# Kernel tuning notes

Measured on AMD Instinct MI355X. Metric: run time of the kernel, lower is better.

## Reference

```python
import jax, jax.numpy as jnp
import numpy as np
from jax import lax

N = 2048
D_ENC = 64      # conv channels
D = 512         # node embedding dim (resnet18 feature dim)
K = 5           # max_num_neighbors
L_LAYERS = 4    # num_layers
ARENA = 32.0    # positions scaled to [0, ARENA)^2
R2 = 2.0        # radius^2 = (sqrt(2))^2


def setup_inputs() -> dict:
    key = jax.random.key(0)
    ks = jax.random.split(key, 9)
    imgs = jax.random.normal(ks[0], (N, 3, 64, 64), dtype=jnp.float32)
    pos = jax.random.uniform(ks[1], (N, 2), dtype=jnp.float32)  # scaled by ARENA inside
    conv_w = jax.random.normal(ks[2], (D_ENC, 3, 7, 7), dtype=jnp.float32) * 0.05
    conv_b = jnp.zeros((D_ENC,), dtype=jnp.float32)
    proj_w = jax.random.normal(ks[3], (D_ENC, D), dtype=jnp.float32) * (1.0 / np.sqrt(D_ENC))
    proj_b = jnp.zeros((D,), dtype=jnp.float32)
    w_self = jax.random.normal(ks[4], (L_LAYERS, D, D), dtype=jnp.float32) * (1.0 / np.sqrt(D))
    w_nbr = jax.random.normal(ks[5], (L_LAYERS, D, D), dtype=jnp.float32) * (1.0 / np.sqrt(D))
    b_gnn = jnp.zeros((L_LAYERS, D), dtype=jnp.float32)
    return {"imgs": imgs, "pos": pos, "conv_w": conv_w, "conv_b": conv_b,
            "proj_w": proj_w, "proj_b": proj_b,
            "w_self": w_self, "w_nbr": w_nbr, "b_gnn": b_gnn}


def _encode(imgs, conv_w, conv_b, proj_w, proj_b):
    # conv 7x7 stride 2 + relu + global avg pool + linear -> [N, D]
    x = lax.conv_general_dilated(imgs, conv_w, window_strides=(2, 2), padding="SAME",
                                 dimension_numbers=("NCHW", "OIHW", "NCHW"))
    x = jax.nn.relu(x + conv_b[None, :, None, None])
    x = x.mean(axis=(2, 3))                      # [N, D_ENC]
    return jax.nn.relu(x @ proj_w + proj_b)      # [N, D]


def _radius_knn(pos):
    # radius graph with radius sqrt(2), no self loops, capped at K neighbors
    p = pos * ARENA                              # [N, 2]
    d2 = jnp.sum((p[:, None, :] - p[None, :, :]) ** 2, axis=-1)  # [N, N]
    invalid = (d2 > R2) | jnp.eye(N, dtype=bool)
    d2m = jnp.where(invalid, jnp.inf, d2)
    neg_vals, idx = lax.top_k(-d2m, K)           # K nearest within radius
    valid = jnp.isfinite(neg_vals)               # [N, K]
    return idx, valid


def reference(imgs, pos, conv_w, conv_b, proj_w, proj_b, w_self, w_nbr, b_gnn):
    h = _encode(imgs, conv_w, conv_b, proj_w, proj_b)   # [N, D]
    idx, valid = _radius_knn(pos)                        # [N, K], [N, K]
    vmask = valid.astype(h.dtype)                        # [N, K]
    denom = jnp.maximum(vmask.sum(axis=1, keepdims=True), 1.0)  # [N, 1]
    for l in range(L_LAYERS):
        nbr = h[idx] * vmask[:, :, None]                 # [N, K, D] gather
        agg = nbr.sum(axis=1) / denom                    # mean over valid neighbors
        h = jax.nn.relu(h @ w_self[l] + agg @ w_nbr[l] + b_gnn[l])
    return h
```

## Files before the change

### kernel.cpp

```cpp
#include <hip/hip_runtime.h>


#define NNODES 2048

typedef __attribute__((ext_vector_type(8))) _Float16 half8;
typedef __attribute__((ext_vector_type(16))) float f32x16;

__device__ inline uint pack2h(float x, float y) {
  ushort a = __builtin_bit_cast(ushort, (_Float16)x);
  ushort b = __builtin_bit_cast(ushort, (_Float16)y);
  return (uint)a | ((uint)b << 16);
}

__global__ __launch_bounds__(256) void setup_kernel(
    const float* __restrict__ conv_w, const float* __restrict__ wsrc_s,
    const float* __restrict__ wsrc_n, const float* __restrict__ pos,
    ushort* __restrict__ wfrag, ushort* __restrict__ wT,
    int* __restrict__ nbr, float* __restrict__ den, float* __restrict__ enc) {
  __shared__ float4 smem4[1040];
  const int bid = blockIdx.x;
  const int tid = threadIdx.x;

  if (bid < 48) {
    int i = bid * 256 + tid;
    int j = i & 7;
    int l = (i >> 3) & 63;
    int q = i >> 9;
    int kb = q % 12, ct = q / 12;
    int g = 2 * kb + (l >> 5);
    int c = 32 * ct + (l & 31);
    float val = 0.f;
    if (g < 21 && j < 7) val = conv_w[c * 147 + g * 7 + j];
    wfrag[i] = __builtin_bit_cast(ushort, (_Float16)val);
    return;
  }

  if (bid < 560) {
    float(*s)[65] = (float(*)[65])smem4;
    int bid2 = bid - 48;
    int m = bid2 >> 6, kt = (bid2 >> 3) & 7, nt = bid2 & 7;
    const float* in = (m < 4) ? (wsrc_s + m * 262144) : (wsrc_n + (m - 4) * 262144);
    ushort* out = wT + m * 262144;
    int k0 = kt << 6, n0 = nt << 6;
#pragma unroll
    for (int rep = 0; rep < 4; ++rep) {
      int row = (rep << 4) + (tid >> 4);
      int c4 = (tid & 15) << 2;
      float4 v = *(const float4*)&in[(k0 + row) * 512 + n0 + c4];
      s[row][c4] = v.x; s[row][c4 + 1] = v.y; s[row][c4 + 2] = v.z; s[row][c4 + 3] = v.w;
    }
    __syncthreads();
#pragma unroll
    for (int rep = 0; rep < 4; ++rep) {
      int n = (rep << 4) + (tid >> 4);
      int k4 = (tid & 15) << 2;
      ushort4 o;
      o.x = __builtin_bit_cast(ushort, (_Float16)s[k4 + 0][n]);
      o.y = __builtin_bit_cast(ushort, (_Float16)s[k4 + 1][n]);
      o.z = __builtin_bit_cast(ushort, (_Float16)s[k4 + 2][n]);
      o.w = __builtin_bit_cast(ushort, (_Float16)s[k4 + 3][n]);
      *(ushort4*)&out[(n0 + n) * 512 + k0 + k4] = o;
    }
    return;
  }

  {
    float* s_d2 = (float*)smem4;
    int* s_idx = (int*)(s_d2 + NNODES);
    int* s_cnt = (int*)(s_idx + NNODES);
    const int i = bid - 560;
    if (tid < 16) {
      float4 z4 = {0.f, 0.f, 0.f, 0.f};
      ((float4*)(enc + i * 64))[tid] = z4;
    }
    if (tid == 0) *s_cnt = 0;
    __syncthreads();
    const float px = pos[2 * i] * 32.f, py = pos[2 * i + 1] * 32.f;
#pragma unroll
    for (int r = 0; r < 8; ++r) {
      int j = tid + (r << 8);
      float2 q = ((const float2*)pos)[j];
      float dx = q.x * 32.f - px, dy = q.y * 32.f - py;
      float d2 = dx * dx + dy * dy;
      if (d2 <= 2.0f && j != i) {
        int slot = atomicAdd(s_cnt, 1);
        s_d2[slot] = d2;
        s_idx[slot] = j;
      }
    }
    __syncthreads();
    if (tid < 64) {
      const int lane = tid;
      const int cnt = *s_cnt;
      int nf = 0;
#pragma unroll
      for (int k = 0; k < 5; ++k) {
        float best = 1e30f;
        int bslot = 0x7fffffff;
        for (int e = lane; e < cnt; e += 64) {
          float d = s_d2[e];
          if (d < best) { best = d; bslot = e; }
        }
#pragma unroll
        for (int off = 1; off < 64; off <<= 1) {
          float od = __shfl_xor(best, off);
          int os = __shfl_xor(bslot, off);
          if (od < best || (od == best && os < bslot)) { best = od; bslot = os; }
        }
        bool got = (best < 1e30f);
        if (lane == 0) nbr[i * 5 + k] = got ? s_idx[bslot] : -1;
        if (got) { s_d2[bslot] = 1e30f; ++nf; }
      }
      if (lane == 0) den[i] = 1.f / (float)(nf > 0 ? nf : 1);
    }
  }
}

__global__ __launch_bounds__(256, 3) void conv_pool_kernel(
    const float* __restrict__ imgs, const ushort* __restrict__ wfrag,
    const float* __restrict__ cb, float* __restrict__ enc) {
  __shared__ int4 s_all[2599];
  ushort* s_img = (ushort*)s_all;
  const half8* swf8 = (const half8*)((char*)s_all + 15984);
  float* s_pool = (float*)((char*)s_all + 40560);

  const int n = blockIdx.x >> 1;
  const int r0half = blockIdx.x & 1;
  const int wy = 32 * r0half - 2;
  const int tid = threadIdx.x;
  const int lane = tid & 63;
  const int w = tid >> 6;
  const int hi = lane >> 5;
  const int lo = lane & 31;

  int4 z = {0, 0, 0, 0};
  for (int i = tid; i < 999; i += 256) s_all[i] = z;
  __syncthreads();

  const int4* wf4 = (const int4*)wfrag;
  int4* swf4 = (int4*)((char*)s_all + 15984);
#pragma unroll
  for (int r = 0; r < 6; ++r) swf4[tid + r * 256] = wf4[tid + r * 256];

  const float4* src = (const float4*)(imgs + (size_t)n * 12288);
  for (int i = tid; i < 1776; i += 256) {
    int ic = i / 592;
    int rem = i - ic * 592;
    int li = rem >> 4, xq = rem & 15;
    int iy = wy + li;
    if (iy >= 0 && iy < 64) {
      float4 v = src[(ic * 64 + iy) * 16 + xq];
      int d = (ic * 37 + li) * 72 + (xq << 2) + 2;
      ((uint*)s_img)[d >> 1] = pack2h(v.x, v.y);
      ((uint*)s_img)[(d >> 1) + 1] = pack2h(v.z, v.w);
    }
  }

  int aoff[12];
#pragma unroll
  for (int kb = 0; kb < 12; ++kb) {
    int g = 2 * kb + hi;
    if (g > 20) g = 20;
    int ic = g / 7, ky = g - ic * 7;
    aoff[kb] = (ic * 37 + ky) * 144 + 4 * lo + w * 1152;
  }
  const float bias0 = cb[lo];
  const float bias1 = cb[32 + lo];
  float pool0 = 0.f, pool1 = 0.f;
  __syncthreads();

  const char* sb = (const char*)s_img;
  union F { half8 v; uint u[4]; };

#define LOADF(F0, F1, B0, B1, KB, TPADD) do {                       \
    const char* p_ = sb + aoff[KB] + (TPADD);                       \
    F0.u[0] = *(const uint*)(p_);       F0.u[1] = *(const uint*)(p_ + 4);   \
    F0.u[2] = *(const uint*)(p_ + 8);   F0.u[3] = *(const uint*)(p_ + 12);  \
    F1.u[0] = *(const uint*)(p_ + 288); F1.u[1] = *(const uint*)(p_ + 292); \
    F1.u[2] = *(const uint*)(p_ + 296); F1.u[3] = *(const uint*)(p_ + 300); \
    B0 = swf8[(KB) * 64 + lane];        B1 = swf8[(12 + (KB)) * 64 + lane]; \
  } while (0)

#pragma unroll
  for (int tp = 0; tp < 2; ++tp) {
    const int tpadd = tp * 576;
    f32x16 a0 = {}, a1 = {}, a2 = {}, a3 = {};
    F f0a, f1a, f0b, f1b;
    half8 b0a, b1a, b0b, b1b;
    LOADF(f0a, f1a, b0a, b1a, 0, tpadd);
#pragma unroll
    for (int kb = 0; kb < 12; kb += 2) {
      LOADF(f0b, f1b, b0b, b1b, kb + 1, tpadd);
      a0 = __builtin_amdgcn_mfma_f32_32x32x16_f16(f0a.v, b0a, a0, 0, 0, 0);
      a1 = __builtin_amdgcn_mfma_f32_32x32x16_f16(f0a.v, b1a, a1, 0, 0, 0);
      a2 = __builtin_amdgcn_mfma_f32_32x32x16_f16(f1a.v, b0a, a2, 0, 0, 0);
      a3 = __builtin_amdgcn_mfma_f32_32x32x16_f16(f1a.v, b1a, a3, 0, 0, 0);
      if (kb + 2 < 12) LOADF(f0a, f1a, b0a, b1a, kb + 2, tpadd);
      a0 = __builtin_amdgcn_mfma_f32_32x32x16_f16(f0b.v, b0b, a0, 0, 0, 0);
      a1 = __builtin_amdgcn_mfma_f32_32x32x16_f16(f0b.v, b1b, a1, 0, 0, 0);
      a2 = __builtin_amdgcn_mfma_f32_32x32x16_f16(f1b.v, b0b, a2, 0, 0, 0);
      a3 = __builtin_amdgcn_mfma_f32_32x32x16_f16(f1b.v, b1b, a3, 0, 0, 0);
    }
    float s0 = 0.f, s1 = 0.f;
#pragma unroll
    for (int r = 0; r < 16; ++r) {
      s0 += fmaxf(a0[r] + bias0, 0.f) + fmaxf(a2[r] + bias0, 0.f);
      s1 += fmaxf(a1[r] + bias1, 0.f) + fmaxf(a3[r] + bias1, 0.f);
    }
    pool0 += s0;
    pool1 += s1;
  }
#undef LOADF

  pool0 += __shfl_xor(pool0, 32);
  pool1 += __shfl_xor(pool1, 32);
  if (lane < 32) {
    s_pool[w * 64 + lo] = pool0;
    s_pool[w * 64 + 32 + lo] = pool1;
  }
  __syncthreads();
  if (tid < 64) {
    float s = s_pool[tid] + s_pool[64 + tid] + s_pool[128 + tid] + s_pool[192 + tid];
    atomicAdd(&enc[n * 64 + tid], s * (1.f / 1024.f));
  }
}

__global__ __launch_bounds__(256) void proj_kernel(
    const float* __restrict__ enc, const float* __restrict__ pw,
    const float* __restrict__ pb, ushort* __restrict__ h16) {
  int c = ((blockIdx.x & 1) << 8) | threadIdx.x;
  int r0 = (blockIdx.x >> 1) << 3;
  float bias = pb[c];
  float acc[8];
#pragma unroll
  for (int r = 0; r < 8; ++r) acc[r] = bias;
#pragma unroll 4
  for (int k = 0; k < 64; ++k) {
    float w = pw[k * 512 + c];
#pragma unroll
    for (int r = 0; r < 8; ++r) acc[r] = fmaf(enc[(r0 + r) * 64 + k], w, acc[r]);
  }
#pragma unroll
  for (int r = 0; r < 8; ++r)
    h16[(r0 + r) * 512 + c] = __builtin_bit_cast(ushort, (_Float16)fmaxf(acc[r], 0.f));
}

__global__ __launch_bounds__(256) void gnn_gemm_kernel(
    const ushort* __restrict__ h16, const int* __restrict__ nbr,
    const float* __restrict__ den,
    const ushort* __restrict__ Ws, const ushort* __restrict__ Wn,
    const float* __restrict__ bias, ushort* __restrict__ hout,
    float* __restrict__ fout, int final_layer) {
  __shared__ ushort s_lds[2][16384];
  __shared__ int s_nbr[320];
  __shared__ float s_den[64];
  const int tid = threadIdx.x;
  const int lane = tid & 63;
  const int hi = lane >> 5, lo = lane & 31;
  const int wu = __builtin_amdgcn_readfirstlane(tid >> 6);
  const int wr = wu >> 1, wc = wu & 1;
  const int bm = blockIdx.x >> 3, bn = blockIdx.x & 7;
  const int r0 = bm << 6, c0 = bn << 6;

  if (tid < 80) ((int4*)s_nbr)[tid] = ((const int4*)(nbr + r0 * 5))[tid];
  else if (tid < 96) ((float4*)s_den)[tid - 80] = ((const float4*)(den + r0))[tid - 80];
  __syncthreads();

  const int grow = tid >> 2, gseg = tid & 3;
  int gj[5];
  uint gm[5];
#pragma unroll
  for (int k = 0; k < 5; ++k) {
    int j = s_nbr[grow * 5 + k];
    gm[k] = (j >= 0) ? 0xFFFFFFFFu : 0u;
    gj[k] = (j >= 0) ? j : 0;
  }
  half8 den8;
  {
    _Float16 dh = (_Float16)s_den[grow];
#pragma unroll
    for (int e = 0; e < 8; ++e) den8[e] = dh;
  }

  union GU { half8 v; uint u[4]; };
  GU ga[5][2];

  auto GATHER = [&](int it) {
    const ushort* hb = h16 + (it << 6) + gseg * 16;
#pragma unroll
    for (int k = 0; k < 5; ++k) {
      const half8* p = (const half8*)(hb + gj[k] * 512);
      ga[k][0].v = p[0];
      ga[k][1].v = p[1];
    }
  };
  auto COMBINE = [&](int buf) {
#pragma unroll
    for (int part = 0; part < 2; ++part) {
      GU t0, t1, t2, t3, t4;
#pragma unroll
      for (int j2 = 0; j2 < 4; ++j2) {
        t0.u[j2] = ga[0][part].u[j2] & gm[0];
        t1.u[j2] = ga[1][part].u[j2] & gm[1];
        t2.u[j2] = ga[2][part].u[j2] & gm[2];
        t3.u[j2] = ga[3][part].u[j2] & gm[3];
        t4.u[j2] = ga[4][part].u[j2] & gm[4];
      }
      half8 s = ((t0.v + t1.v) + (t2.v + t3.v)) + t4.v;
      s = s * den8;
      *(half8*)&s_lds[buf][4096 + (2 * gseg + part) * 512 + grow * 8] = s;
    }
  };
  auto STAGE = [&](int buf, int it) {
    int k0 = it << 6;
    const ushort* ph = h16 + (r0 + lane) * 512 + k0 + 8 * wu;
    const ushort* ps = Ws + (c0 + lane) * 512 + k0 + 8 * wu;
    const ushort* pn = Wn + (c0 + lane) * 512 + k0 + 8 * wu;
    ushort* lb = &s_lds[buf][wu << 9];
#define GLDS(SRC, DST) __builtin_amdgcn_global_load_lds( \
      (const __attribute__((address_space(1))) void*)(SRC), \
      (__attribute__((address_space(3))) void*)(DST), 16, 0, 0)
    GLDS(ph, lb);            GLDS(ph + 32, lb + 2048);
    GLDS(ps, lb + 8192);     GLDS(ps + 32, lb + 10240);
    GLDS(pn, lb + 12288);    GLDS(pn + 32, lb + 14336);
#undef GLDS
  };

  f32x16 accS = {}, accN = {};
  GATHER(0);
  STAGE(0, 0);
  COMBINE(0);
  __syncthreads();
  int cur = 0;
  for (int it = 0; it < 8; ++it) {
    if (it < 7) {
      GATHER(it + 1);
      STAGE(cur ^ 1, it + 1);
    }
    const half8* pAh = (const half8*)&s_lds[cur][0];
    const half8* pAg = (const half8*)&s_lds[cur][4096];
    const half8* pBs = (const half8*)&s_lds[cur][8192];
    const half8* pBn = (const half8*)&s_lds[cur][12288];
#pragma unroll
    for (int ks = 0; ks < 4; ++ks) {
      int gi = (2 * ks + hi) * 64;
      half8 ah = pAh[gi + 32 * wr + lo];
      half8 bs = pBs[gi + 32 * wc + lo];
      accS = __builtin_amdgcn_mfma_f32_32x32x16_f16(ah, bs, accS, 0, 0, 0);
      half8 ag = pAg[gi + 32 * wr + lo];
      half8 bn2 = pBn[gi + 32 * wc + lo];
      accN = __builtin_amdgcn_mfma_f32_32x32x16_f16(ag, bn2, accN, 0, 0, 0);
    }
    if (it < 7) COMBINE(cur ^ 1);
    __syncthreads();
    cur ^= 1;
  }

  const int col = c0 + 32 * wc + lo;
  const float b = bias[col];
#pragma unroll
  for (int r = 0; r < 16; ++r) {
    int row = r0 + 32 * wr + (r & 3) + ((r >> 2) << 3) + (hi << 2);
    float v = fmaxf(accS[r] + accN[r] + b, 0.f);
    if (final_layer) fout[row * 512 + col] = v;
    else hout[row * 512 + col] = __builtin_bit_cast(ushort, (_Float16)v);
  }
}

extern "C" void kernel_launch(void* const* d_in, const int* in_sizes, int n_in,
                              void* d_out, int out_size, void* d_ws, size_t ws_size,
                              hipStream_t stream) {
  const float* imgs   = (const float*)d_in[0];
  const float* pos    = (const float*)d_in[1];
  const float* conv_w = (const float*)d_in[2];
  const float* conv_b = (const float*)d_in[3];
  const float* proj_w = (const float*)d_in[4];
  const float* proj_b = (const float*)d_in[5];
  const float* w_self = (const float*)d_in[6];
  const float* w_nbr  = (const float*)d_in[7];
  const float* b_gnn  = (const float*)d_in[8];

  char* ws = (char*)d_ws;
  ushort* wfrag = (ushort*)(ws);
  float*  enc   = (float*) (ws + 32768);
  ushort* h16a  = (ushort*)(ws + 557056);
  ushort* h16b  = (ushort*)(ws + 2654208);
  ushort* wT16  = (ushort*)(ws + 6848512);
  int*    nbr   = (int*)   (ws + 11042816);
  float*  den   = (float*) (ws + 11083776);

  setup_kernel<<<2608, 256, 0, stream>>>(conv_w, w_self, w_nbr, pos,
                                         wfrag, wT16, nbr, den, enc);
  conv_pool_kernel<<<2 * NNODES, 256, 0, stream>>>(imgs, wfrag, conv_b, enc);
  proj_kernel<<<512, 256, 0, stream>>>(enc, proj_w, proj_b, h16a);

  for (int l = 0; l < 4; ++l) {
    ushort* hin  = (l & 1) ? h16b : h16a;
    ushort* hnew = (l & 1) ? h16a : h16b;
    gnn_gemm_kernel<<<256, 256, 0, stream>>>(
        hin, nbr, den, wT16 + l * 262144, wT16 + (4 + l) * 262144,
        b_gnn + l * 512, hnew, (float*)d_out, (l == 3) ? 1 : 0);
  }
}
```

Before: 141.7 us.

## Split GNN GEMM K-loop across two wave groups with LDS reduction

The GNN layer kernel now launches 512 threads per block. Two groups of four waves each process half of the K dimension with their own double-buffered LDS stages, and the partial accumulators are reduced through LDS before the epilogue. The aim is more waves per block and a shorter serial K-loop, since only 256 blocks run on a GPU with many CUs. The cost is doubled LDS (128KB), which limits occupancy, plus an extra reduction barrier. Separately, the conv fragment loads are rewritten as 8-byte memcpy loads with an alignment hint so the compiler may emit wider LDS reads.

```diff
diff --git a/kernel.cpp b/kernel.cpp
--- a/kernel.cpp
+++ b/kernel.cpp
@@ -172,13 +172,14 @@
   const char* sb = (const char*)s_img;
   union F { half8 v; uint u[4]; };
 
-#define LOADF(F0, F1, B0, B1, KB, TPADD) do {                       \
-    const char* p_ = sb + aoff[KB] + (TPADD);                       \
-    F0.u[0] = *(const uint*)(p_);       F0.u[1] = *(const uint*)(p_ + 4);   \
-    F0.u[2] = *(const uint*)(p_ + 8);   F0.u[3] = *(const uint*)(p_ + 12);  \
-    F1.u[0] = *(const uint*)(p_ + 288); F1.u[1] = *(const uint*)(p_ + 292); \
-    F1.u[2] = *(const uint*)(p_ + 296); F1.u[3] = *(const uint*)(p_ + 300); \
-    B0 = swf8[(KB) * 64 + lane];        B1 = swf8[(12 + (KB)) * 64 + lane]; \
+#define LOADF(F0, F1, B0, B1, KB, TPADD) do {                                 \
+    const char* p_ = (const char*)__builtin_assume_aligned(                   \
+        sb + aoff[KB] + (TPADD), 4);                                          \
+    __builtin_memcpy(&F0.u[0], p_, 8);                                        \
+    __builtin_memcpy(&F0.u[2], p_ + 8, 8);                                    \
+    __builtin_memcpy(&F1.u[0], p_ + 288, 8);                                  \
+    __builtin_memcpy(&F1.u[2], p_ + 296, 8);                                  \
+    B0 = swf8[(KB) * 64 + lane];        B1 = swf8[(12 + (KB)) * 64 + lane];   \
   } while (0)
 
 #pragma unroll
@@ -245,28 +246,31 @@
     h16[(r0 + r) * 512 + c] = __builtin_bit_cast(ushort, (_Float16)fmaxf(acc[r], 0.f));
 }
 
-__global__ __launch_bounds__(256) void gnn_gemm_kernel(
+__global__ __launch_bounds__(512) void gnn_gemm_kernel(
     const ushort* __restrict__ h16, const int* __restrict__ nbr,
     const float* __restrict__ den,
     const ushort* __restrict__ Ws, const ushort* __restrict__ Wn,
     const float* __restrict__ bias, ushort* __restrict__ hout,
     float* __restrict__ fout, int final_layer) {
-  __shared__ ushort s_lds[2][16384];
+  __shared__ ushort s_lds[4][16384];
   __shared__ int s_nbr[320];
   __shared__ float s_den[64];
   const int tid = threadIdx.x;
   const int lane = tid & 63;
   const int hi = lane >> 5, lo = lane & 31;
-  const int wu = __builtin_amdgcn_readfirstlane(tid >> 6);
-  const int wr = wu >> 1, wc = wu & 1;
+  const int grp = tid >> 8;
+  const int wug = __builtin_amdgcn_readfirstlane((tid >> 6) & 3);
+  const int wr = wug >> 1, wc = wug & 1;
   const int bm = blockIdx.x >> 3, bn = blockIdx.x & 7;
   const int r0 = bm << 6, c0 = bn << 6;
+  const int itb = grp << 2;
 
   if (tid < 80) ((int4*)s_nbr)[tid] = ((const int4*)(nbr + r0 * 5))[tid];
   else if (tid < 96) ((float4*)s_den)[tid - 80] = ((const float4*)(den + r0))[tid - 80];
   __syncthreads();
 
-  const int grow = tid >> 2, gseg = tid & 3;
+  const int ltid = tid & 255;
+  const int grow = ltid >> 2, gseg = ltid & 3;
   int gj[5];
   uint gm[5];
 #pragma unroll
@@ -313,10 +317,10 @@
   };
   auto STAGE = [&](int buf, int it) {
     int k0 = it << 6;
-    const ushort* ph = h16 + (r0 + lane) * 512 + k0 + 8 * wu;
-    const ushort* ps = Ws + (c0 + lane) * 512 + k0 + 8 * wu;
-    const ushort* pn = Wn + (c0 + lane) * 512 + k0 + 8 * wu;
-    ushort* lb = &s_lds[buf][wu << 9];
+    const ushort* ph = h16 + (r0 + lane) * 512 + k0 + 8 * wug;
+    const ushort* ps = Ws + (c0 + lane) * 512 + k0 + 8 * wug;
+    const ushort* pn = Wn + (c0 + lane) * 512 + k0 + 8 * wug;
+    ushort* lb = &s_lds[buf][wug << 9];
 #define GLDS(SRC, DST) __builtin_amdgcn_global_load_lds( \
       (const __attribute__((address_space(1))) void*)(SRC), \
       (__attribute__((address_space(3))) void*)(DST), 16, 0, 0)
@@ -327,20 +331,21 @@
   };
 
   f32x16 accS = {}, accN = {};
-  GATHER(0);
-  STAGE(0, 0);
-  COMBINE(0);
+  GATHER(itb);
+  STAGE(itb == 0 ? 0 : 2, itb);
+  COMBINE(itb == 0 ? 0 : 2);
   __syncthreads();
   int cur = 0;
-  for (int it = 0; it < 8; ++it) {
-    if (it < 7) {
-      GATHER(it + 1);
-      STAGE(cur ^ 1, it + 1);
-    }
-    const half8* pAh = (const half8*)&s_lds[cur][0];
-    const half8* pAg = (const half8*)&s_lds[cur][4096];
-    const half8* pBs = (const half8*)&s_lds[cur][8192];
-    const half8* pBn = (const half8*)&s_lds[cur][12288];
+  const int bufbase = grp << 1;
+  for (int it = 0; it < 4; ++it) {
+    if (it < 3) {
+      GATHER(itb + it + 1);
+      STAGE(bufbase + (cur ^ 1), itb + it + 1);
+    }
+    const half8* pAh = (const half8*)&s_lds[bufbase + cur][0];
+    const half8* pAg = (const half8*)&s_lds[bufbase + cur][4096];
+    const half8* pBs = (const half8*)&s_lds[bufbase + cur][8192];
+    const half8* pBn = (const half8*)&s_lds[bufbase + cur][12288];
 #pragma unroll
     for (int ks = 0; ks < 4; ++ks) {
       int gi = (2 * ks + hi) * 64;
@@ -351,19 +356,28 @@
       half8 bn2 = pBn[gi + 32 * wc + lo];
       accN = __builtin_amdgcn_mfma_f32_32x32x16_f16(ag, bn2, accN, 0, 0, 0);
     }
-    if (it < 7) COMBINE(cur ^ 1);
+    if (it < 3) COMBINE(bufbase + (cur ^ 1));
     __syncthreads();
     cur ^= 1;
   }
 
-  const int col = c0 + 32 * wc + lo;
-  const float b = bias[col];
-#pragma unroll
-  for (int r = 0; r < 16; ++r) {
-    int row = r0 + 32 * wr + (r & 3) + ((r >> 2) << 3) + (hi << 2);
-    float v = fmaxf(accS[r] + accN[r] + b, 0.f);
-    if (final_layer) fout[row * 512 + col] = v;
-    else hout[row * 512 + col] = __builtin_bit_cast(ushort, (_Float16)v);
+  float* s_red = (float*)&s_lds[0][0];
+  if (grp == 1) {
+#pragma unroll
+    for (int r = 0; r < 16; ++r)
+      s_red[(ltid << 4) + r] = accS[r] + accN[r];
+  }
+  __syncthreads();
+  if (grp == 0) {
+    const int col = c0 + 32 * wc + lo;
+    const float b = bias[col];
+#pragma unroll
+    for (int r = 0; r < 16; ++r) {
+      int row = r0 + 32 * wr + (r & 3) + ((r >> 2) << 3) + (hi << 2);
+      float v = fmaxf(accS[r] + accN[r] + s_red[(ltid << 4) + r] + b, 0.f);
+      if (final_layer) fout[row * 512 + col] = v;
+      else hout[row * 512 + col] = __builtin_bit_cast(ushort, (_Float16)v);
+    }
   }
 }
 
@@ -397,7 +411,7 @@
   for (int l = 0; l < 4; ++l) {
     ushort* hin  = (l & 1) ? h16b : h16a;
     ushort* hnew = (l & 1) ? h16a : h16b;
-    gnn_gemm_kernel<<<256, 256, 0, stream>>>(
+    gnn_gemm_kernel<<<256, 512, 0, stream>>>(
         hin, nbr, den, wT16 + l * 262144, wT16 + (4 + l) * 262144,
         b_gnn + l * 512, hnew, (float*)d_out, (l == 3) ? 1 : 0);
   }
```

New measurement: 140.1 us. Within noise of the previous version (-1.2%).
